# Optimization experiments

Hardware: AMD Instinct MI355X
Metric: run time of the kernel (lower is better)

The kernel has to match this reference:

```python
import jax, jax.numpy as jnp
import numpy as np

B, T, IN, H, OUT = 16384, 200, 9, 64, 3


def setup_inputs() -> dict:
    key = jax.random.key(0)
    ks = jax.random.split(key, 12)
    s_in, s_h = 1.0 / np.sqrt(H), 1.0 / np.sqrt(H)  # torch LSTMCell init scale = 1/sqrt(hidden)
    u = lambda k, shape: jax.random.uniform(k, shape, jnp.float32, -s_h, s_h)
    return {
        "x": jax.random.normal(ks[0], (B, T, IN), jnp.float32),
        "W_ih1": u(ks[1], (4 * H, IN)),
        "W_hh1": u(ks[2], (4 * H, H)),
        "b_ih1": u(ks[3], (4 * H,)),
        "b_hh1": u(ks[4], (4 * H,)),
        "W_ih2": u(ks[5], (4 * H, H)),
        "W_hh2": u(ks[6], (4 * H, H)),
        "b_ih2": u(ks[7], (4 * H,)),
        "b_hh2": u(ks[8], (4 * H,)),
        "W_out": u(ks[9], (OUT, H)),
        "b_out": u(ks[10], (OUT,)),
    }


def _lstm_cell(x, h, c, W_ih, W_hh, b_ih, b_hh):
    # PyTorch gate order: i, f, g, o
    gates = x @ W_ih.T + b_ih + h @ W_hh.T + b_hh  # [B, 4H]
    i, f, g, o = jnp.split(gates, 4, axis=-1)
    i, f, o = jax.nn.sigmoid(i), jax.nn.sigmoid(f), jax.nn.sigmoid(o)
    g = jnp.tanh(g)
    c_new = f * c + i * g
    h_new = o * jnp.tanh(c_new)
    return h_new, c_new


def reference(x, W_ih1, W_hh1, b_ih1, b_hh1, W_ih2, W_hh2, b_ih2, b_hh2, W_out, b_out):
    batch = x.shape[0]
    hdim = W_hh1.shape[1]
    zeros = jnp.zeros((batch, hdim), x.dtype)
    init = (zeros, zeros, zeros, zeros)  # h1, c1, h2, c2

    def step(carry, x_t):
        h1, c1, h2, c2 = carry
        h1, c1 = _lstm_cell(x_t, h1, c1, W_ih1, W_hh1, b_ih1, b_hh1)
        h2, c2 = _lstm_cell(h1, h2, c2, W_ih2, W_hh2, b_ih2, b_hh2)
        return (h1, c1, h2, c2), None

    (h1, c1, h2, c2), _ = jax.lax.scan(step, init, jnp.swapaxes(x, 0, 1))  # scan over time
    out = h2 @ W_out.T + b_out  # [B, OUT]
    return out[:, None, :]  # [B, 1, OUT]
```

## Files before the change

kernel.cpp:

```cpp
#include <hip/hip_runtime.h>
#include <hip/hip_bf16.h>


#define B_TOT   16384
#define T_STEPS 200
#define IN_DIM  9
#define HDIM    64

#define PK1_OFF 0
#define PK2_OFF 24576
#define BSUM_HALF_OFF 57344
#define PACK_W_TOT 57344
#define PACK_TOT (PACK_W_TOT + 512)

#define L2E     1.44269504089f
#define TWOL2E  2.88539008178f

typedef _Float16 half8 __attribute__((ext_vector_type(8)));
typedef float    f32x4 __attribute__((ext_vector_type(4)));
typedef float    f4u   __attribute__((ext_vector_type(4), aligned(4)));

__global__ void pack_kernel(const float* __restrict__ Wih1, const float* __restrict__ Whh1,
                            const float* __restrict__ bih1, const float* __restrict__ bhh1,
                            const float* __restrict__ Wih2, const float* __restrict__ Whh2,
                            const float* __restrict__ bih2, const float* __restrict__ bhh2,
                            float* __restrict__ ws) {
    int e = blockIdx.x * 256 + threadIdx.x;
    if (e >= PACK_TOT) return;
    _Float16* wh = (_Float16*)ws;
    float* bptr = (float*)(wh + BSUM_HALF_OFF);
    auto gscale = [](int q) -> float {
        int gt = q >> 6;
        return (gt == 2) ? (-2.0f * L2E) : -L2E;
    };
    if (e < PK2_OFF) {
        int j = e & 7, lane = (e >> 3) & 63, nt = (e >> 9) & 15, c = e >> 13;
        int k = c * 32 + 4 * (lane >> 4) + (j & 3) + 16 * (j >> 2);
        int q = nt * 16 + (lane & 15);
        float v = 0.0f;
        if (k < 64)      v = Whh1[q * 64 + k];
        else if (k < 73) v = Wih1[q * 9 + (k - 64)];
        wh[e] = (_Float16)(v * gscale(q));
    } else if (e < PACK_W_TOT) {
        int e2 = e - PK2_OFF;
        int j = e2 & 7, lane = (e2 >> 3) & 63, nt = (e2 >> 9) & 15, c = e2 >> 13;
        int k = c * 32 + 4 * (lane >> 4) + (j & 3) + 16 * (j >> 2);
        int q = nt * 16 + (lane & 15);
        float v = (k < 64) ? Wih2[q * 64 + k] : Whh2[q * 64 + (k - 64)];
        wh[e] = (_Float16)(v * gscale(q));
    } else if (e < PACK_W_TOT + 256) {
        int q = e - PACK_W_TOT;
        bptr[q] = (bih1[q] + bhh1[q]) * gscale(q);
    } else {
        int q = e - PACK_W_TOT - 256;
        bptr[256 + q] = (bih2[q] + bhh2[q]) * gscale(q);
    }
}

__global__ __launch_bounds__(256, 2) void lstm_mfma(
    const float* __restrict__ x,
    const float* __restrict__ ws_f,
    const float* __restrict__ Wout,
    const float* __restrict__ bout,
    float* __restrict__ out)
{
    const int tid  = threadIdx.x;
    const int lane = tid & 63;
    const int w    = __builtin_amdgcn_readfirstlane(tid >> 6);
    const int l15  = lane & 15;
    const int l4   = lane >> 4;

    const _Float16* wh  = (const _Float16*)ws_f;
    const _Float16* pk1 = wh + PK1_OFF;
    const _Float16* pk2 = wh + PK2_OFF;
    const float* bsum   = (const float*)(wh + BSUM_HALF_OFF);

    __shared__ _Float16 h1s[2][16][72];
    __shared__ _Float16 h2s[2][16][72];

    for (int i = tid; i < 2 * 16 * 72; i += 256) {
        (&h1s[0][0][0])[i] = (_Float16)0.0f;
        (&h2s[0][0][0])[i] = (_Float16)0.0f;
    }
    __syncthreads();

    const int bbase = blockIdx.x * 16;
    const float* xb = x + (long)(bbase + l15) * (T_STEPS * IN_DIM);

    f4u  cx  = {0.f, 0.f, 0.f, 0.f};
    float cx8 = 0.0f;
    auto prefetch_x = [&](int tt) {
        const float* xp = xb + tt * IN_DIM;
        if (l4 < 2)       cx  = *(const f4u*)(xp + 4 * l4);
        else if (l4 == 2) cx8 = xp[8];
    };
    auto build_ax = [&]() -> half8 {
        half8 ax;
        float e0 = (l4 == 2) ? cx8 : cx[0];
        ax[0] = (_Float16)e0;    ax[1] = (_Float16)cx[1];
        ax[2] = (_Float16)cx[2]; ax[3] = (_Float16)cx[3];
        ax[4] = ax[5] = ax[6] = ax[7] = (_Float16)0.0f;
        return ax;
    };

    half8 bw1_00, bw1_01, bw1_02, bw1_03;
    half8 bw1_10, bw1_11, bw1_12, bw1_13;
    half8 bw1_20, bw1_21, bw1_22, bw1_23;
    half8 bw2_00, bw2_01, bw2_02, bw2_03;
    half8 bw2_10, bw2_11, bw2_12, bw2_13;
    half8 bw2_20, bw2_21, bw2_22, bw2_23;
    half8 bw2_30, bw2_31, bw2_32, bw2_33;
    {
        #define LD1(c,g) *(const half8*)(pk1 + (((c * 16) + (w + 4 * g)) * 64 + lane) * 8)
        #define LD2(c,g) *(const half8*)(pk2 + (((c * 16) + (w + 4 * g)) * 64 + lane) * 8)
        bw1_00 = LD1(0,0); bw1_01 = LD1(0,1); bw1_02 = LD1(0,2); bw1_03 = LD1(0,3);
        bw1_10 = LD1(1,0); bw1_11 = LD1(1,1); bw1_12 = LD1(1,2); bw1_13 = LD1(1,3);
        bw1_20 = LD1(2,0); bw1_21 = LD1(2,1); bw1_22 = LD1(2,2); bw1_23 = LD1(2,3);
        bw2_00 = LD2(0,0); bw2_01 = LD2(0,1); bw2_02 = LD2(0,2); bw2_03 = LD2(0,3);
        bw2_10 = LD2(1,0); bw2_11 = LD2(1,1); bw2_12 = LD2(1,2); bw2_13 = LD2(1,3);
        bw2_20 = LD2(2,0); bw2_21 = LD2(2,1); bw2_22 = LD2(2,2); bw2_23 = LD2(2,3);
        bw2_30 = LD2(3,0); bw2_31 = LD2(3,1); bw2_32 = LD2(3,2); bw2_33 = LD2(3,3);
        #undef LD1
        #undef LD2
    }

    float bias1[4], bias2[4];
    #pragma unroll
    for (int g = 0; g < 4; ++g) {
        bias1[g] = bsum[(w + 4 * g) * 16 + l15];
        bias2[g] = bsum[256 + (w + 4 * g) * 16 + l15];
    }

    const int hpos = ((w >> 1) << 5) + 8 * (l15 >> 2) + (l15 & 3) + ((w & 1) << 2);

    f32x4 c1 = {0.f, 0.f, 0.f, 0.f};
    f32x4 c2 = {0.f, 0.f, 0.f, 0.f};

    auto cell_update = [&](f32x4* G, f32x4& cs, _Float16* hb) {
        #pragma unroll
        for (int r = 0; r < 4; ++r) {
            float ei = __builtin_amdgcn_exp2f(G[0][r]);
            float ef = __builtin_amdgcn_exp2f(G[1][r]);
            float eg = __builtin_amdgcn_exp2f(G[2][r]);
            float eo = __builtin_amdgcn_exp2f(G[3][r]);
            float ai = 1.0f + ei, af = 1.0f + ef, ag = 1.0f + eg;
            float gm = 1.0f - eg;
            float pp = ai * ag;
            float num = __builtin_fmaf(gm, af, cs[r] * pp);
            float den = af * pp;
            float cc  = num * __builtin_amdgcn_rcpf(den);
            cs[r] = cc;
            float z  = cc * TWOL2E;
            int   zi = __float_as_int(z);
            float ec = __builtin_amdgcn_exp2f(__int_as_float(zi | (int)0x80000000));
            float tm = 1.0f - ec;
            float d2 = (1.0f + eo) * (1.0f + ec);
            float hs = __int_as_float(__float_as_int(tm) ^ (zi & (int)0x80000000));
            float hv = hs * __builtin_amdgcn_rcpf(d2);
            hb[(4 * l4 + r) * 72 + hpos] = (_Float16)hv;
        }
    };

    prefetch_x(0);
    f32x4 C[4];
    {
        half8 ax0 = build_ax();
        #pragma unroll
        for (int g = 0; g < 4; ++g) C[g] = (f32x4){bias1[g], bias1[g], bias1[g], bias1[g]};
        C[0] = __builtin_amdgcn_mfma_f32_16x16x32_f16(ax0, bw1_20, C[0], 0, 0, 0);
        C[1] = __builtin_amdgcn_mfma_f32_16x16x32_f16(ax0, bw1_21, C[1], 0, 0, 0);
        C[2] = __builtin_amdgcn_mfma_f32_16x16x32_f16(ax0, bw1_22, C[2], 0, 0, 0);
        C[3] = __builtin_amdgcn_mfma_f32_16x16x32_f16(ax0, bw1_23, C[3], 0, 0, 0);
    }
    prefetch_x(1);

    int p = 0;
    for (int t = 0; t < T_STEPS; ++t) {
        asm volatile("" :
            "+v"(bw1_00), "+v"(bw1_01), "+v"(bw1_02), "+v"(bw1_03),
            "+v"(bw1_10), "+v"(bw1_11), "+v"(bw1_12), "+v"(bw1_13),
            "+v"(bw1_20), "+v"(bw1_21), "+v"(bw1_22), "+v"(bw1_23));
        asm volatile("" :
            "+v"(bw2_00), "+v"(bw2_01), "+v"(bw2_02), "+v"(bw2_03),
            "+v"(bw2_10), "+v"(bw2_11), "+v"(bw2_12), "+v"(bw2_13),
            "+v"(bw2_20), "+v"(bw2_21), "+v"(bw2_22), "+v"(bw2_23),
            "+v"(bw2_30), "+v"(bw2_31), "+v"(bw2_32), "+v"(bw2_33),
            "+v"(bias1[0]), "+v"(bias1[1]), "+v"(bias1[2]), "+v"(bias1[3]),
            "+v"(bias2[0]), "+v"(bias2[1]), "+v"(bias2[2]), "+v"(bias2[3]));

        cell_update(C, c1, &h1s[1 - p][0][0]);

        __syncthreads();

        half8 a10  = *(const half8*)&h1s[1 - p][l15][ 0 + 8 * l4];
        half8 a11  = *(const half8*)&h1s[1 - p][l15][32 + 8 * l4];
        half8 a2h0 = *(const half8*)&h2s[p][l15][ 0 + 8 * l4];
        half8 a2h1 = *(const half8*)&h2s[p][l15][32 + 8 * l4];
        half8 ax   = build_ax();
        int nt = t + 2; if (nt > T_STEPS - 1) nt = T_STEPS - 1;
        prefetch_x(nt);

        f32x4 D[4];
        #pragma unroll
        for (int g = 0; g < 4; ++g) D[g] = (f32x4){bias2[g], bias2[g], bias2[g], bias2[g]};
        D[0] = __builtin_amdgcn_mfma_f32_16x16x32_f16(a10,  bw2_00, D[0], 0, 0, 0);
        D[1] = __builtin_amdgcn_mfma_f32_16x16x32_f16(a10,  bw2_01, D[1], 0, 0, 0);
        D[2] = __builtin_amdgcn_mfma_f32_16x16x32_f16(a10,  bw2_02, D[2], 0, 0, 0);
        D[3] = __builtin_amdgcn_mfma_f32_16x16x32_f16(a10,  bw2_03, D[3], 0, 0, 0);
        D[0] = __builtin_amdgcn_mfma_f32_16x16x32_f16(a11,  bw2_10, D[0], 0, 0, 0);
        D[1] = __builtin_amdgcn_mfma_f32_16x16x32_f16(a11,  bw2_11, D[1], 0, 0, 0);
        D[2] = __builtin_amdgcn_mfma_f32_16x16x32_f16(a11,  bw2_12, D[2], 0, 0, 0);
        D[3] = __builtin_amdgcn_mfma_f32_16x16x32_f16(a11,  bw2_13, D[3], 0, 0, 0);
        D[0] = __builtin_amdgcn_mfma_f32_16x16x32_f16(a2h0, bw2_20, D[0], 0, 0, 0);
        D[1] = __builtin_amdgcn_mfma_f32_16x16x32_f16(a2h0, bw2_21, D[1], 0, 0, 0);
        D[2] = __builtin_amdgcn_mfma_f32_16x16x32_f16(a2h0, bw2_22, D[2], 0, 0, 0);
        D[3] = __builtin_amdgcn_mfma_f32_16x16x32_f16(a2h0, bw2_23, D[3], 0, 0, 0);
        D[0] = __builtin_amdgcn_mfma_f32_16x16x32_f16(a2h1, bw2_30, D[0], 0, 0, 0);
        D[1] = __builtin_amdgcn_mfma_f32_16x16x32_f16(a2h1, bw2_31, D[1], 0, 0, 0);
        D[2] = __builtin_amdgcn_mfma_f32_16x16x32_f16(a2h1, bw2_32, D[2], 0, 0, 0);
        D[3] = __builtin_amdgcn_mfma_f32_16x16x32_f16(a2h1, bw2_33, D[3], 0, 0, 0);

        f32x4 Cn[4];
        #pragma unroll
        for (int g = 0; g < 4; ++g) Cn[g] = (f32x4){bias1[g], bias1[g], bias1[g], bias1[g]};
        Cn[0] = __builtin_amdgcn_mfma_f32_16x16x32_f16(a10, bw1_00, Cn[0], 0, 0, 0);
        Cn[1] = __builtin_amdgcn_mfma_f32_16x16x32_f16(a10, bw1_01, Cn[1], 0, 0, 0);
        Cn[2] = __builtin_amdgcn_mfma_f32_16x16x32_f16(a10, bw1_02, Cn[2], 0, 0, 0);
        Cn[3] = __builtin_amdgcn_mfma_f32_16x16x32_f16(a10, bw1_03, Cn[3], 0, 0, 0);
        Cn[0] = __builtin_amdgcn_mfma_f32_16x16x32_f16(a11, bw1_10, Cn[0], 0, 0, 0);
        Cn[1] = __builtin_amdgcn_mfma_f32_16x16x32_f16(a11, bw1_11, Cn[1], 0, 0, 0);
        Cn[2] = __builtin_amdgcn_mfma_f32_16x16x32_f16(a11, bw1_12, Cn[2], 0, 0, 0);
        Cn[3] = __builtin_amdgcn_mfma_f32_16x16x32_f16(a11, bw1_13, Cn[3], 0, 0, 0);
        Cn[0] = __builtin_amdgcn_mfma_f32_16x16x32_f16(ax,  bw1_20, Cn[0], 0, 0, 0);
        Cn[1] = __builtin_amdgcn_mfma_f32_16x16x32_f16(ax,  bw1_21, Cn[1], 0, 0, 0);
        Cn[2] = __builtin_amdgcn_mfma_f32_16x16x32_f16(ax,  bw1_22, Cn[2], 0, 0, 0);
        Cn[3] = __builtin_amdgcn_mfma_f32_16x16x32_f16(ax,  bw1_23, Cn[3], 0, 0, 0);

        cell_update(D, c2, &h2s[1 - p][0][0]);

        #pragma unroll
        for (int g = 0; g < 4; ++g) C[g] = Cn[g];
        p ^= 1;
    }
    __syncthreads();

    if (tid < 48) {
        int bl = tid / 3, o = tid - bl * 3;
        float acc = bout[o];
        #pragma unroll 8
        for (int pos = 0; pos < HDIM; ++pos) {
            int sub = pos & 31;
            int j = (pos >> 5) * 32 + (((sub >> 2) & 1) << 4) + ((sub >> 3) << 2) + (sub & 3);
            acc = __builtin_fmaf(Wout[o * 64 + j], (float)h2s[0][bl][pos], acc);
        }
        out[(bbase + bl) * 3 + o] = acc;
    }
}

extern "C" void kernel_launch(void* const* d_in, const int* in_sizes, int n_in,
                              void* d_out, int out_size, void* d_ws, size_t ws_size,
                              hipStream_t stream) {
    const float* x     = (const float*)d_in[0];
    const float* Wih1  = (const float*)d_in[1];
    const float* Whh1  = (const float*)d_in[2];
    const float* bih1  = (const float*)d_in[3];
    const float* bhh1  = (const float*)d_in[4];
    const float* Wih2  = (const float*)d_in[5];
    const float* Whh2  = (const float*)d_in[6];
    const float* bih2  = (const float*)d_in[7];
    const float* bhh2  = (const float*)d_in[8];
    const float* Wout  = (const float*)d_in[9];
    const float* bout  = (const float*)d_in[10];
    float* ws  = (float*)d_ws;
    float* out = (float*)d_out;

    pack_kernel<<<(PACK_TOT + 255) / 256, 256, 0, stream>>>(
        Wih1, Whh1, bih1, bhh1, Wih2, Whh2, bih2, bhh2, ws);

    lstm_mfma<<<B_TOT / 16, 256, 0, stream>>>(x, ws, Wout, bout, out);
}
```

Before: 597.4 us.

## Stage x windows in LDS, unroll time loop by two, batch reciprocals

Input x is now loaded cooperatively by all threads in 8-step windows, converted to fp16, and double-buffered in shared memory, so each step no longer issues a per-lane global load and conversion. The time loop is unrolled by two with fixed LDS buffer indices, which removes the ping-pong index arithmetic. The cell update shares one reciprocal across four denominators with a product trick, cutting rcp instructions. This adds LDS traffic, slightly changes numerics, and relies on T being even.

```diff
diff --git a/kernel.cpp b/kernel.cpp
--- a/kernel.cpp
+++ b/kernel.cpp
@@ -16,9 +16,10 @@
 #define L2E     1.44269504089f
 #define TWOL2E  2.88539008178f
 
-typedef _Float16 half8 __attribute__((ext_vector_type(8)));
-typedef float    f32x4 __attribute__((ext_vector_type(4)));
-typedef float    f4u   __attribute__((ext_vector_type(4), aligned(4)));
+typedef _Float16 half8  __attribute__((ext_vector_type(8)));
+typedef _Float16 half4v __attribute__((ext_vector_type(4)));
+typedef float    f32x4  __attribute__((ext_vector_type(4)));
+typedef float    f4u    __attribute__((ext_vector_type(4), aligned(4)));
 
 __global__ void pack_kernel(const float* __restrict__ Wih1, const float* __restrict__ Whh1,
                             const float* __restrict__ bih1, const float* __restrict__ bhh1,
@@ -77,30 +78,53 @@
 
     __shared__ _Float16 h1s[2][16][72];
     __shared__ _Float16 h2s[2][16][72];
+    __shared__ _Float16 xwin[2][8][4][16][4];
 
     for (int i = tid; i < 2 * 16 * 72; i += 256) {
         (&h1s[0][0][0])[i] = (_Float16)0.0f;
         (&h2s[0][0][0])[i] = (_Float16)0.0f;
     }
-    __syncthreads();
+    for (int i = tid; i < 2 * 8 * 4 * 16 * 4; i += 256)
+        (&xwin[0][0][0][0][0])[i] = (_Float16)0.0f;
 
     const int bbase = blockIdx.x * 16;
-    const float* xb = x + (long)(bbase + l15) * (T_STEPS * IN_DIM);
-
-    f4u  cx  = {0.f, 0.f, 0.f, 0.f};
-    float cx8 = 0.0f;
-    auto prefetch_x = [&](int tt) {
-        const float* xp = xb + tt * IN_DIM;
-        if (l4 < 2)       cx  = *(const f4u*)(xp + 4 * l4);
-        else if (l4 == 2) cx8 = xp[8];
-    };
-    auto build_ax = [&]() -> half8 {
-        half8 ax;
-        float e0 = (l4 == 2) ? cx8 : cx[0];
-        ax[0] = (_Float16)e0;    ax[1] = (_Float16)cx[1];
-        ax[2] = (_Float16)cx[2]; ax[3] = (_Float16)cx[3];
-        ax[4] = ax[5] = ax[6] = ax[7] = (_Float16)0.0f;
-        return ax;
+
+    const int b_ = tid & 15, z_ = tid >> 4;
+    const int s0_ = (z_ * 11) >> 5, q0_ = z_ - 3 * s0_;
+    const bool act1 = (z_ < 8);
+    const int pz1 = z_ + 16;
+    const int s1_ = (pz1 * 11) >> 5, q1_ = pz1 - 3 * s1_;
+    const float* xbL = x + (long)(bbase + b_) * (T_STEPS * IN_DIM);
+
+    f4u pfA = {0.f, 0.f, 0.f, 0.f}, pfB = {0.f, 0.f, 0.f, 0.f};
+    auto fetch_x = [&](int wb) {
+        int t0 = wb + s0_; if (t0 > T_STEPS - 1) t0 = T_STEPS - 1;
+        const float* p0 = xbL + t0 * IN_DIM + 4 * q0_;
+        if (q0_ < 2) pfA = *(const f4u*)p0; else pfA[0] = p0[0];
+        if (act1) {
+            int t1 = wb + s1_; if (t1 > T_STEPS - 1) t1 = T_STEPS - 1;
+            const float* p1 = xbL + t1 * IN_DIM + 4 * q1_;
+            if (q1_ < 2) pfB = *(const f4u*)p1; else pfB[0] = p1[0];
+        }
+    };
+    auto store_x = [&](int buf) {
+        f4u A = pfA, B = pfB;
+        if (q0_ == 2) { A[1] = 0.f; A[2] = 0.f; A[3] = 0.f; }
+        half4v hv;
+        hv[0] = (_Float16)A[0]; hv[1] = (_Float16)A[1];
+        hv[2] = (_Float16)A[2]; hv[3] = (_Float16)A[3];
+        *(half4v*)&xwin[buf][s0_][q0_][b_][0] = hv;
+        if (act1) {
+            if (q1_ == 2) { B[1] = 0.f; B[2] = 0.f; B[3] = 0.f; }
+            half4v hw;
+            hw[0] = (_Float16)B[0]; hw[1] = (_Float16)B[1];
+            hw[2] = (_Float16)B[2]; hw[3] = (_Float16)B[3];
+            *(half4v*)&xwin[buf][s1_][q1_][b_][0] = hw;
+        }
+    };
+    auto read_ax = [&](int tt) -> half8 {
+        half4v xq = *(const half4v*)&xwin[(tt >> 3) & 1][tt & 7][l4][l15][0];
+        return __builtin_shufflevector(xq, xq, 0, 1, 2, 3, 0, 1, 2, 3);
     };
 
     half8 bw1_00, bw1_01, bw1_02, bw1_03;
@@ -137,34 +161,68 @@
     f32x4 c2 = {0.f, 0.f, 0.f, 0.f};
 
     auto cell_update = [&](f32x4* G, f32x4& cs, _Float16* hb) {
+        float num[4], den[4], eo4[4], d2[4], hs4[4];
         #pragma unroll
         for (int r = 0; r < 4; ++r) {
             float ei = __builtin_amdgcn_exp2f(G[0][r]);
             float ef = __builtin_amdgcn_exp2f(G[1][r]);
             float eg = __builtin_amdgcn_exp2f(G[2][r]);
-            float eo = __builtin_amdgcn_exp2f(G[3][r]);
+            eo4[r]   = __builtin_amdgcn_exp2f(G[3][r]);
             float ai = 1.0f + ei, af = 1.0f + ef, ag = 1.0f + eg;
             float gm = 1.0f - eg;
             float pp = ai * ag;
-            float num = __builtin_fmaf(gm, af, cs[r] * pp);
-            float den = af * pp;
-            float cc  = num * __builtin_amdgcn_rcpf(den);
+            num[r] = __builtin_fmaf(gm, af, cs[r] * pp);
+            den[r] = af * pp;
+        }
+        float s01 = den[0] * den[1], s23 = den[2] * den[3];
+        float Pinv = __builtin_amdgcn_rcpf(s01 * s23);
+        float r01 = Pinv * s23, r23 = Pinv * s01;
+        float inv0 = r01 * den[1], inv1 = r01 * den[0];
+        float inv2 = r23 * den[3], inv3 = r23 * den[2];
+        float inv[4] = {inv0, inv1, inv2, inv3};
+        #pragma unroll
+        for (int r = 0; r < 4; ++r) {
+            float cc = num[r] * inv[r];
             cs[r] = cc;
             float z  = cc * TWOL2E;
             int   zi = __float_as_int(z);
             float ec = __builtin_amdgcn_exp2f(__int_as_float(zi | (int)0x80000000));
             float tm = 1.0f - ec;
-            float d2 = (1.0f + eo) * (1.0f + ec);
-            float hs = __int_as_float(__float_as_int(tm) ^ (zi & (int)0x80000000));
-            float hv = hs * __builtin_amdgcn_rcpf(d2);
-            hb[(4 * l4 + r) * 72 + hpos] = (_Float16)hv;
-        }
-    };
-
-    prefetch_x(0);
+            d2[r] = (1.0f + eo4[r]) * (1.0f + ec);
+            hs4[r] = __int_as_float(__float_as_int(tm) ^ (zi & (int)0x80000000));
+        }
+        float t01 = d2[0] * d2[1], t23 = d2[2] * d2[3];
+        float Qinv = __builtin_amdgcn_rcpf(t01 * t23);
+        float q01 = Qinv * t23, q23 = Qinv * t01;
+        float jnv[4] = {q01 * d2[1], q01 * d2[0], q23 * d2[3], q23 * d2[2]};
+        #pragma unroll
+        for (int r = 0; r < 4; ++r)
+            hb[(4 * l4 + r) * 72 + hpos] = (_Float16)(hs4[r] * jnv[r]);
+    };
+
+    #define PIN_ALL() do {                                                      \
+        asm volatile("" :                                                       \
+            "+v"(bw1_00), "+v"(bw1_01), "+v"(bw1_02), "+v"(bw1_03),             \
+            "+v"(bw1_10), "+v"(bw1_11), "+v"(bw1_12), "+v"(bw1_13),             \
+            "+v"(bw1_20), "+v"(bw1_21), "+v"(bw1_22), "+v"(bw1_23));            \
+        asm volatile("" :                                                       \
+            "+v"(bw2_00), "+v"(bw2_01), "+v"(bw2_02), "+v"(bw2_03),             \
+            "+v"(bw2_10), "+v"(bw2_11), "+v"(bw2_12), "+v"(bw2_13),             \
+            "+v"(bw2_20), "+v"(bw2_21), "+v"(bw2_22), "+v"(bw2_23),             \
+            "+v"(bw2_30), "+v"(bw2_31), "+v"(bw2_32), "+v"(bw2_33),             \
+            "+v"(bias1[0]), "+v"(bias1[1]), "+v"(bias1[2]), "+v"(bias1[3]),     \
+            "+v"(bias2[0]), "+v"(bias2[1]), "+v"(bias2[2]), "+v"(bias2[3]));    \
+    } while (0)
+
+    fetch_x(0);
+    __syncthreads();
+    store_x(0);
+    fetch_x(8);
+    __syncthreads();
+
     f32x4 C[4];
     {
-        half8 ax0 = build_ax();
+        half8 ax0 = read_ax(0);
         #pragma unroll
         for (int g = 0; g < 4; ++g) C[g] = (f32x4){bias1[g], bias1[g], bias1[g], bias1[g]};
         C[0] = __builtin_amdgcn_mfma_f32_16x16x32_f16(ax0, bw1_20, C[0], 0, 0, 0);
@@ -172,33 +230,21 @@
         C[2] = __builtin_amdgcn_mfma_f32_16x16x32_f16(ax0, bw1_22, C[2], 0, 0, 0);
         C[3] = __builtin_amdgcn_mfma_f32_16x16x32_f16(ax0, bw1_23, C[3], 0, 0, 0);
     }
-    prefetch_x(1);
-
-    int p = 0;
-    for (int t = 0; t < T_STEPS; ++t) {
-        asm volatile("" :
-            "+v"(bw1_00), "+v"(bw1_01), "+v"(bw1_02), "+v"(bw1_03),
-            "+v"(bw1_10), "+v"(bw1_11), "+v"(bw1_12), "+v"(bw1_13),
-            "+v"(bw1_20), "+v"(bw1_21), "+v"(bw1_22), "+v"(bw1_23));
-        asm volatile("" :
-            "+v"(bw2_00), "+v"(bw2_01), "+v"(bw2_02), "+v"(bw2_03),
-            "+v"(bw2_10), "+v"(bw2_11), "+v"(bw2_12), "+v"(bw2_13),
-            "+v"(bw2_20), "+v"(bw2_21), "+v"(bw2_22), "+v"(bw2_23),
-            "+v"(bw2_30), "+v"(bw2_31), "+v"(bw2_32), "+v"(bw2_33),
-            "+v"(bias1[0]), "+v"(bias1[1]), "+v"(bias1[2]), "+v"(bias1[3]),
-            "+v"(bias2[0]), "+v"(bias2[1]), "+v"(bias2[2]), "+v"(bias2[3]));
-
-        cell_update(C, c1, &h1s[1 - p][0][0]);
-
+
+    for (int t = 0; t < T_STEPS; t += 2) {
+        PIN_ALL();
+        cell_update(C, c1, &h1s[1][0][0]);
+        if ((t & 7) == 0) {
+            store_x(((t >> 3) + 1) & 1);
+            fetch_x(t + 16);
+        }
         __syncthreads();
 
-        half8 a10  = *(const half8*)&h1s[1 - p][l15][ 0 + 8 * l4];
-        half8 a11  = *(const half8*)&h1s[1 - p][l15][32 + 8 * l4];
-        half8 a2h0 = *(const half8*)&h2s[p][l15][ 0 + 8 * l4];
-        half8 a2h1 = *(const half8*)&h2s[p][l15][32 + 8 * l4];
-        half8 ax   = build_ax();
-        int nt = t + 2; if (nt > T_STEPS - 1) nt = T_STEPS - 1;
-        prefetch_x(nt);
+        half8 a10  = *(const half8*)&h1s[1][l15][ 0 + 8 * l4];
+        half8 a11  = *(const half8*)&h1s[1][l15][32 + 8 * l4];
+        half8 a2h0 = *(const half8*)&h2s[0][l15][ 0 + 8 * l4];
+        half8 a2h1 = *(const half8*)&h2s[0][l15][32 + 8 * l4];
+        half8 ax   = read_ax(t + 1);
 
         f32x4 D[4];
         #pragma unroll
@@ -220,27 +266,70 @@
         D[2] = __builtin_amdgcn_mfma_f32_16x16x32_f16(a2h1, bw2_32, D[2], 0, 0, 0);
         D[3] = __builtin_amdgcn_mfma_f32_16x16x32_f16(a2h1, bw2_33, D[3], 0, 0, 0);
 
-        f32x4 Cn[4];
-        #pragma unroll
-        for (int g = 0; g < 4; ++g) Cn[g] = (f32x4){bias1[g], bias1[g], bias1[g], bias1[g]};
-        Cn[0] = __builtin_amdgcn_mfma_f32_16x16x32_f16(a10, bw1_00, Cn[0], 0, 0, 0);
-        Cn[1] = __builtin_amdgcn_mfma_f32_16x16x32_f16(a10, bw1_01, Cn[1], 0, 0, 0);
-        Cn[2] = __builtin_amdgcn_mfma_f32_16x16x32_f16(a10, bw1_02, Cn[2], 0, 0, 0);
-        Cn[3] = __builtin_amdgcn_mfma_f32_16x16x32_f16(a10, bw1_03, Cn[3], 0, 0, 0);
-        Cn[0] = __builtin_amdgcn_mfma_f32_16x16x32_f16(a11, bw1_10, Cn[0], 0, 0, 0);
-        Cn[1] = __builtin_amdgcn_mfma_f32_16x16x32_f16(a11, bw1_11, Cn[1], 0, 0, 0);
-        Cn[2] = __builtin_amdgcn_mfma_f32_16x16x32_f16(a11, bw1_12, Cn[2], 0, 0, 0);
-        Cn[3] = __builtin_amdgcn_mfma_f32_16x16x32_f16(a11, bw1_13, Cn[3], 0, 0, 0);
-        Cn[0] = __builtin_amdgcn_mfma_f32_16x16x32_f16(ax,  bw1_20, Cn[0], 0, 0, 0);
-        Cn[1] = __builtin_amdgcn_mfma_f32_16x16x32_f16(ax,  bw1_21, Cn[1], 0, 0, 0);
-        Cn[2] = __builtin_amdgcn_mfma_f32_16x16x32_f16(ax,  bw1_22, Cn[2], 0, 0, 0);
-        Cn[3] = __builtin_amdgcn_mfma_f32_16x16x32_f16(ax,  bw1_23, Cn[3], 0, 0, 0);
-
-        cell_update(D, c2, &h2s[1 - p][0][0]);
-
-        #pragma unroll
-        for (int g = 0; g < 4; ++g) C[g] = Cn[g];
-        p ^= 1;
+        f32x4 CB[4];
+        #pragma unroll
+        for (int g = 0; g < 4; ++g) CB[g] = (f32x4){bias1[g], bias1[g], bias1[g], bias1[g]};
+        CB[0] = __builtin_amdgcn_mfma_f32_16x16x32_f16(a10, bw1_00, CB[0], 0, 0, 0);
+        CB[1] = __builtin_amdgcn_mfma_f32_16x16x32_f16(a10, bw1_01, CB[1], 0, 0, 0);
+        CB[2] = __builtin_amdgcn_mfma_f32_16x16x32_f16(a10, bw1_02, CB[2], 0, 0, 0);
+        CB[3] = __builtin_amdgcn_mfma_f32_16x16x32_f16(a10, bw1_03, CB[3], 0, 0, 0);
+        CB[0] = __builtin_amdgcn_mfma_f32_16x16x32_f16(a11, bw1_10, CB[0], 0, 0, 0);
+        CB[1] = __builtin_amdgcn_mfma_f32_16x16x32_f16(a11, bw1_11, CB[1], 0, 0, 0);
+        CB[2] = __builtin_amdgcn_mfma_f32_16x16x32_f16(a11, bw1_12, CB[2], 0, 0, 0);
+        CB[3] = __builtin_amdgcn_mfma_f32_16x16x32_f16(a11, bw1_13, CB[3], 0, 0, 0);
+        CB[0] = __builtin_amdgcn_mfma_f32_16x16x32_f16(ax,  bw1_20, CB[0], 0, 0, 0);
+        CB[1] = __builtin_amdgcn_mfma_f32_16x16x32_f16(ax,  bw1_21, CB[1], 0, 0, 0);
+        CB[2] = __builtin_amdgcn_mfma_f32_16x16x32_f16(ax,  bw1_22, CB[2], 0, 0, 0);
+        CB[3] = __builtin_amdgcn_mfma_f32_16x16x32_f16(ax,  bw1_23, CB[3], 0, 0, 0);
+
+        cell_update(D, c2, &h2s[1][0][0]);
+
+        PIN_ALL();
+        cell_update(CB, c1, &h1s[0][0][0]);
+        __syncthreads();
+
+        half8 b10  = *(const half8*)&h1s[0][l15][ 0 + 8 * l4];
+        half8 b11  = *(const half8*)&h1s[0][l15][32 + 8 * l4];
+        half8 b2h0 = *(const half8*)&h2s[1][l15][ 0 + 8 * l4];
+        half8 b2h1 = *(const half8*)&h2s[1][l15][32 + 8 * l4];
+        half8 bx   = read_ax(t + 2);
+
+        f32x4 E[4];
+        #pragma unroll
+        for (int g = 0; g < 4; ++g) E[g] = (f32x4){bias2[g], bias2[g], bias2[g], bias2[g]};
+        E[0] = __builtin_amdgcn_mfma_f32_16x16x32_f16(b10,  bw2_00, E[0], 0, 0, 0);
+        E[1] = __builtin_amdgcn_mfma_f32_16x16x32_f16(b10,  bw2_01, E[1], 0, 0, 0);
+        E[2] = __builtin_amdgcn_mfma_f32_16x16x32_f16(b10,  bw2_02, E[2], 0, 0, 0);
+        E[3] = __builtin_amdgcn_mfma_f32_16x16x32_f16(b10,  bw2_03, E[3], 0, 0, 0);
+        E[0] = __builtin_amdgcn_mfma_f32_16x16x32_f16(b11,  bw2_10, E[0], 0, 0, 0);
+        E[1] = __builtin_amdgcn_mfma_f32_16x16x32_f16(b11,  bw2_11, E[1], 0, 0, 0);
+        E[2] = __builtin_amdgcn_mfma_f32_16x16x32_f16(b11,  bw2_12, E[2], 0, 0, 0);
+        E[3] = __builtin_amdgcn_mfma_f32_16x16x32_f16(b11,  bw2_13, E[3], 0, 0, 0);
+        E[0] = __builtin_amdgcn_mfma_f32_16x16x32_f16(b2h0, bw2_20, E[0], 0, 0, 0);
+        E[1] = __builtin_amdgcn_mfma_f32_16x16x32_f16(b2h0, bw2_21, E[1], 0, 0, 0);
+        E[2] = __builtin_amdgcn_mfma_f32_16x16x32_f16(b2h0, bw2_22, E[2], 0, 0, 0);
+        E[3] = __builtin_amdgcn_mfma_f32_16x16x32_f16(b2h0, bw2_23, E[3], 0, 0, 0);
+        E[0] = __builtin_amdgcn_mfma_f32_16x16x32_f16(b2h1, bw2_30, E[0], 0, 0, 0);
+        E[1] = __builtin_amdgcn_mfma_f32_16x16x32_f16(b2h1, bw2_31, E[1], 0, 0, 0);
+        E[2] = __builtin_amdgcn_mfma_f32_16x16x32_f16(b2h1, bw2_32, E[2], 0, 0, 0);
+        E[3] = __builtin_amdgcn_mfma_f32_16x16x32_f16(b2h1, bw2_33, E[3], 0, 0, 0);
+
+        #pragma unroll
+        for (int g = 0; g < 4; ++g) C[g] = (f32x4){bias1[g], bias1[g], bias1[g], bias1[g]};
+        C[0] = __builtin_amdgcn_mfma_f32_16x16x32_f16(b10, bw1_00, C[0], 0, 0, 0);
+        C[1] = __builtin_amdgcn_mfma_f32_16x16x32_f16(b10, bw1_01, C[1], 0, 0, 0);
+        C[2] = __builtin_amdgcn_mfma_f32_16x16x32_f16(b10, bw1_02, C[2], 0, 0, 0);
+        C[3] = __builtin_amdgcn_mfma_f32_16x16x32_f16(b10, bw1_03, C[3], 0, 0, 0);
+        C[0] = __builtin_amdgcn_mfma_f32_16x16x32_f16(b11, bw1_10, C[0], 0, 0, 0);
+        C[1] = __builtin_amdgcn_mfma_f32_16x16x32_f16(b11, bw1_11, C[1], 0, 0, 0);
+        C[2] = __builtin_amdgcn_mfma_f32_16x16x32_f16(b11, bw1_12, C[2], 0, 0, 0);
+        C[3] = __builtin_amdgcn_mfma_f32_16x16x32_f16(b11, bw1_13, C[3], 0, 0, 0);
+        C[0] = __builtin_amdgcn_mfma_f32_16x16x32_f16(bx,  bw1_20, C[0], 0, 0, 0);
+        C[1] = __builtin_amdgcn_mfma_f32_16x16x32_f16(bx,  bw1_21, C[1], 0, 0, 0);
+        C[2] = __builtin_amdgcn_mfma_f32_16x16x32_f16(bx,  bw1_22, C[2], 0, 0, 0);
+        C[3] = __builtin_amdgcn_mfma_f32_16x16x32_f16(bx,  bw1_23, C[3], 0, 0, 0);
+
+        cell_update(E, c2, &h2s[0][0][0]);
     }
     __syncthreads();
 
@@ -255,6 +344,7 @@
         }
         out[(bbase + bl) * 3 + o] = acc;
     }
+    #undef PIN_ALL
 }
 
 extern "C" void kernel_launch(void* const* d_in, const int* in_sizes, int n_in,
```

Result: faster. 526.4 us (-11.9%).
